# Kernel optimization log

Hardware: AMD Instinct MI355X
Metric: run time of the kernel (lower is better)

The kernel has to match this reference:

```python
import jax, jax.numpy as jnp
import numpy as np

B = 1024      # batch
V = 5023      # FLAME vertices
NF = 9976     # FLAME faces
NJ = 5        # joints: global, neck, jaw, eyeL, eyeR
NL = 51       # static landmarks
PARENTS = (-1, 0, 1, 1, 1)


def setup_inputs() -> dict:
    key = jax.random.key(0)
    ks = jax.random.split(key, 16)
    inp = {}
    # trainable flame parameters (small pose magnitudes for realism)
    inp['shape_params'] = jax.random.normal(ks[0], (B, 300), jnp.float32)
    inp['expression_params'] = jax.random.normal(ks[1], (B, 100), jnp.float32)
    inp['global_rot'] = 0.1 * jax.random.normal(ks[2], (B, 3), jnp.float32)
    inp['neck_pose'] = 0.1 * jax.random.normal(ks[3], (B, 3), jnp.float32)
    inp['jaw_pose'] = 0.1 * jax.random.normal(ks[4], (B, 3), jnp.float32)
    inp['eye_pose'] = 0.1 * jax.random.normal(ks[5], (B, 6), jnp.float32)
    inp['transl'] = jax.random.normal(ks[6], (B, 3), jnp.float32)
    # flame buffers
    inp['v_template'] = jax.random.normal(ks[7], (V, 3), jnp.float32)
    inp['shapedirs'] = 0.01 * jax.random.normal(ks[8], (V, 3, 400), jnp.float32)
    inp['posedirs'] = 0.01 * jax.random.normal(ks[9], (36, V * 3), jnp.float32)
    Jreg = jax.random.uniform(ks[10], (NJ, V), jnp.float32)
    inp['J_regressor'] = Jreg / jnp.sum(Jreg, axis=1, keepdims=True)
    W = jax.random.uniform(ks[11], (V, NJ), jnp.float32)
    inp['lbs_weights'] = W / jnp.sum(W, axis=1, keepdims=True)
    bc = jax.random.uniform(ks[12], (NL, 3), jnp.float32)
    inp['lmk_bary_coords'] = bc / jnp.sum(bc, axis=1, keepdims=True)
    inp['parents'] = jnp.array(PARENTS, dtype=jnp.int32)
    inp['faces'] = jax.random.randint(ks[13], (NF, 3), 0, V, jnp.int32)
    inp['lmk_faces_idx'] = jax.random.randint(ks[14], (NL,), 0, NF, jnp.int64)
    return inp


def batch_rodrigues(rvecs):
    # rvecs: [N,3] axis-angle -> [N,3,3] rotation matrices
    angle = jnp.sqrt(jnp.sum(jnp.square(rvecs + 1e-8), axis=1, keepdims=True))  # [N,1]
    axis = rvecs / angle
    s = jnp.sin(angle)[:, :, None]
    c = jnp.cos(angle)[:, :, None]
    rx, ry, rz = axis[:, 0], axis[:, 1], axis[:, 2]
    zeros = jnp.zeros_like(rx)
    K = jnp.stack([zeros, -rz, ry, rz, zeros, -rx, -ry, rx, zeros], axis=1).reshape(-1, 3, 3)
    I = jnp.eye(3, dtype=rvecs.dtype)
    return I + s * K + (1.0 - c) * (K @ K)


def _lbs(betas, full_pose, v_template, shapedirs, posedirs, J_regressor, lbs_weights):
    b = betas.shape[0]
    # shape+expression blendshapes
    v_shaped = v_template[None] + jnp.einsum('bl,vkl->bvk', betas, shapedirs)  # [B,V,3]
    joints = jnp.einsum('jv,bvk->bjk', J_regressor, v_shaped)                 # [B,J,3]
    rot_mats = batch_rodrigues(full_pose.reshape(-1, 3)).reshape(b, NJ, 3, 3)
    # pose blendshapes (exclude root)
    ident = jnp.eye(3, dtype=betas.dtype)
    pose_feature = (rot_mats[:, 1:] - ident).reshape(b, 9 * (NJ - 1))         # [B,36]
    v_posed = v_shaped + (pose_feature @ posedirs).reshape(b, V, 3)
    # rigid kinematic chain
    rel_joints = jnp.concatenate(
        [joints[:, :1], joints[:, 1:] - joints[:, jnp.array(PARENTS[1:])]], axis=1)
    bottom = jnp.broadcast_to(jnp.array([0., 0., 0., 1.], betas.dtype), (b, NJ, 1, 4))
    tf = jnp.concatenate(
        [jnp.concatenate([rot_mats, rel_joints[..., None]], axis=3), bottom], axis=2)  # [B,J,4,4]
    chain = [tf[:, 0]]
    for i in range(1, NJ):
        chain.append(chain[PARENTS[i]] @ tf[:, i])
    transforms = jnp.stack(chain, axis=1)                                    # [B,J,4,4]
    # remove rest-pose joint location from translation column
    jh = jnp.einsum('bjmn,bjn->bjm', transforms[:, :, :3, :3], joints)       # [B,J,3]
    A = transforms.at[:, :, :3, 3].add(-jh)
    # skinning
    T = jnp.einsum('vj,bjmn->bvmn', lbs_weights, A)                          # [B,V,4,4]
    v_h = jnp.concatenate([v_posed, jnp.ones((b, V, 1), betas.dtype)], axis=2)
    verts = jnp.einsum('bvmn,bvn->bvm', T, v_h)[..., :3]                     # [B,V,3]
    return verts, transforms[:, :, :3, 3]


def reference(shape_params, expression_params, global_rot, neck_pose, jaw_pose,
              eye_pose, transl, v_template, shapedirs, posedirs, J_regressor,
              lbs_weights, lmk_bary_coords, parents, faces, lmk_faces_idx):
    betas = jnp.concatenate([shape_params, expression_params], axis=1)       # [B,400]
    full_pose = jnp.concatenate([global_rot, neck_pose, jaw_pose, eye_pose], axis=1)  # [B,15]
    vertices, _ = _lbs(betas, full_pose, v_template, shapedirs, posedirs,
                       J_regressor, lbs_weights)
    # barycentric landmark interpolation
    lmk_faces = faces[lmk_faces_idx]                                         # [L,3]
    lmk_verts = vertices[:, lmk_faces]                                       # [B,L,3,3]
    landmarks_3d = jnp.einsum('blfk,lf->blk', lmk_verts, lmk_bary_coords)    # [B,L,3]
    landmarks_3d = landmarks_3d + transl[:, None]
    vertices = vertices + transl[:, None]
    # default-weights flame regularizer (fixed_shape=None, ref_vertices=None)
    flame_reg = (100.0 * jnp.sum(neck_pose ** 2)
                 + 0.001 * jnp.sum(jaw_pose ** 2)
                 + 0.001 * jnp.sum(shape_params ** 2)
                 + 0.001 * jnp.sum(expression_params ** 2))
    return vertices, landmarks_3d, flame_reg
```

## Files before the change

### kernel.cpp

```cpp
#include <hip/hip_runtime.h>
#include <hip/hip_bf16.h>

#define BATCH 1024
#define NV 5023
#define NJOINT 5
#define NLMK 51
#define N3 (NV*3)
#define NPADB 15072
#define KBETA 400
#define KTOT 448
#define NSTEP 14
#define RB_B (NPADB/16)
#define RB_A 64
#define FRAG 512

#define BM 64
#define BN 48
#define NVC 128
#define CVT_BLKS 3297

#define GBM 64
#define GBN 192
#define GNP 79
#define GGRID 1280
#define CH_S 52

typedef __attribute__((ext_vector_type(8))) short short8;
typedef __attribute__((ext_vector_type(4))) float floatx4;
typedef __attribute__((ext_vector_type(4))) float float4v;

#define GLDS16(gp, lp) \
    __builtin_amdgcn_global_load_lds( \
        (const __attribute__((address_space(1))) void*)(gp), \
        (__attribute__((address_space(3))) void*)(lp), 16, 0, 0)

#define WS_JS      0
#define WS_BASEJ   24064
#define WS_REG     24512
#define WS_FLAGS   24520
#define WS_AMAT    24576
#define WS_ACT     270336
#define WS_WB      1187840
#define WS_FULL    14692352

__device__ __forceinline__ float ldf(const void* p, long i, int f32) {
    if (f32) return ((const float*)p)[i];
    return __bfloat162float(((const __hip_bfloat16*)p)[i]);
}
__device__ __forceinline__ short8 ld8bf(const void* p, long i, int f32) {
    if (f32) {
        float4v a = *(const float4v*)((const float*)p + i);
        float4v b = *(const float4v*)((const float*)p + i + 4);
        short8 r;
#pragma unroll
        for (int j = 0; j < 4; ++j) {
            __hip_bfloat16 h = __float2bfloat16(a[j]);
            r[j] = *reinterpret_cast<short*>(&h);
        }
#pragma unroll
        for (int j = 0; j < 4; ++j) {
            __hip_bfloat16 h = __float2bfloat16(b[j]);
            r[4 + j] = *reinterpret_cast<short*>(&h);
        }
        return r;
    }
    return *(const short8*)((const __hip_bfloat16*)p + i);
}
__device__ __forceinline__ void stf(void* p, long i, float v, int f32) {
    if (f32) ((float*)p)[i] = v;
    else ((__hip_bfloat16*)p)[i] = __float2bfloat16(v);
}

__device__ __forceinline__ long act2_off(int b, int k) {
    return (((long)(k >> 5) * RB_A + (b >> 4)) * 64 + ((k >> 3) & 3) * 16 + (b & 15)) * 8 + (k & 7);
}

__device__ __forceinline__ int probe_f32(const void* shape_p) {
    int lane = threadIdx.x & 63;
    unsigned short h = ((const unsigned short*)shape_p)[2 * lane];
    union { unsigned short u; __hip_bfloat16 b; } cv; cv.u = h;
    float v = fabsf(__bfloat162float(cv.b));
    if (v != v) v = 3.4e38f;
#pragma unroll
    for (int off = 32; off; off >>= 1) v = fmaxf(v, __shfl_down(v, off));
    v = __shfl(v, 0);
    return v > 1e4f;
}
__device__ __forceinline__ int probe_i64(const void* lmk_idx) {
    int lane = threadIdx.x & 63;
    const int* q = (const int*)lmk_idx;
    int odd_nonzero = (lane < 25) && (q[2*lane + 1] != 0);
    unsigned long long b = __ballot(odd_nonzero);
    return b == 0ull;
}

__global__ void k_init(float* ws0, const void* shape_p, const void* lmk_idx, int* flags) {
    int i = blockIdx.x * 256 + threadIdx.x;
    if (i < 6129) ws0[i] = 0.f;
    if (blockIdx.x == 0 && threadIdx.x < 64) {
        int f = probe_f32(shape_p);
        int i64 = probe_i64(lmk_idx);
        if (threadIdx.x == 0) { flags[0] = f; flags[1] = i64; }
    }
}

__global__ __launch_bounds__(256) void k_prep(const void* __restrict__ shapedirs,
                                              const void* __restrict__ posedirs,
                                              const void* __restrict__ Jreg,
                                              const void* __restrict__ v_template,
                                              const void* __restrict__ shape_p,
                                              float* __restrict__ reg,
                                              __hip_bfloat16* __restrict__ Wb,
                                              float* __restrict__ PART) {
    int f32 = probe_f32(shape_p);
    int blk = blockIdx.x, tid = threadIdx.x;
    if (blk < CVT_BLKS) {
        if (blk == 0 && tid == 0) reg[0] = 0.f;
        int g = blk * 256 + tid;
        int s = g / (RB_B * 64);
        int rem = g - s * (RB_B * 64);
        int R = rem >> 6;
        int l = rem & 63;
        int quad = l >> 4, fr = l & 15;
        int n = R * 16 + fr;
        int k0 = s * 32 + quad * 8;
        short8 o;
#pragma unroll
        for (int e = 0; e < 8; ++e) o[e] = 0;
        if (n < N3) {
            if (k0 < KBETA) {
                o = ld8bf(shapedirs, (long)n * KBETA + k0, f32);
            } else if (k0 < 440) {
#pragma unroll
                for (int e = 0; e < 8; ++e) {
                    int kk = k0 + e - KBETA;
                    float val = (kk < 36) ? ldf(posedirs, (long)kk * N3 + n, f32) : 0.f;
                    __hip_bfloat16 h = __float2bfloat16(val);
                    o[e] = *reinterpret_cast<short*>(&h);
                }
            }
        }
        *(short8*)(Wb + (long)g * 8) = o;
    } else {
        int b2 = blk - CVT_BLKS;
        int k = b2 >> 7;
        int vc = b2 & 127;
        int v0 = vc * 40, v1 = min(NV, v0 + 40);
        int l2 = tid + 256;
        float acc1[NJOINT] = {0,0,0,0,0};
        float acc2[NJOINT] = {0,0,0,0,0};
        for (int v = v0; v < v1; ++v) {
            float s1 = ldf(shapedirs, (long)v*1200 + k*400 + tid, f32);
            float s2 = 0.f;
            if (l2 < 400)       s2 = ldf(shapedirs, (long)v*1200 + k*400 + l2, f32);
            else if (l2 == 400) s2 = ldf(v_template, v*3 + k, f32);
#pragma unroll
            for (int j = 0; j < NJOINT; ++j) {
                float jr = ldf(Jreg, j*NV + v, f32);
                acc1[j] += jr * s1;
                acc2[j] += jr * s2;
            }
        }
        long base = ((long)(k*NVC + vc)*5)*401;
#pragma unroll
        for (int j = 0; j < NJOINT; ++j) {
            PART[base + j*401 + tid] = acc1[j];
            if (l2 <= 400) PART[base + j*401 + l2] = acc2[j];
        }
    }
}

__global__ __launch_bounds__(256) void k_js_red(const float* __restrict__ PART,
                                                float* __restrict__ JS,
                                                float* __restrict__ baseJ) {
    int o = blockIdx.x * 256 + threadIdx.x;
    if (o >= 3*5*401) return;
    int k = o / 2005, r = o - k*2005;
    int j = r / 401, l = r - j*401;
    float s = 0.f;
    long base = ((long)(k*NVC)*5 + j)*401 + l;
    for (int vc = 0; vc < NVC; ++vc) s += PART[base + (long)vc*2005];
    if (l < 400) JS[j*1200 + k*400 + l] = s;
    else         baseJ[j*3 + k] = s;
}

__global__ void k_js_atomic(const void* __restrict__ Jreg,
                            const void* __restrict__ shapedirs,
                            const void* __restrict__ v_template,
                            const int* __restrict__ flags,
                            float* __restrict__ JS, float* __restrict__ baseJ) {
    int f32 = flags[0];
    int k = blockIdx.x, vc = blockIdx.y, tid = threadIdx.x;
    int v0 = vc * 79, v1 = min(NV, v0 + 79);
    int l2 = tid + 256;
    float acc1[NJOINT] = {0,0,0,0,0};
    float acc2[NJOINT] = {0,0,0,0,0};
    for (int v = v0; v < v1; ++v) {
        float s1 = ldf(shapedirs, (long)v*1200 + k*400 + tid, f32);
        float s2 = 0.f;
        if (l2 < 400)       s2 = ldf(shapedirs, (long)v*1200 + k*400 + l2, f32);
        else if (l2 == 400) s2 = ldf(v_template, v*3 + k, f32);
#pragma unroll
        for (int j = 0; j < NJOINT; ++j) {
            float jr = ldf(Jreg, j*NV + v, f32);
            acc1[j] += jr * s1;
            acc2[j] += jr * s2;
        }
    }
#pragma unroll
    for (int j = 0; j < NJOINT; ++j) {
        atomicAdd(&JS[j*1200 + k*400 + tid], acc1[j]);
        if (l2 < 400)       atomicAdd(&JS[j*1200 + k*400 + l2], acc2[j]);
        else if (l2 == 400) atomicAdd(&baseJ[j*3 + k], acc2[j]);
    }
}

__global__ __launch_bounds__(64) void k_batch(
        const void* __restrict__ shape_p, const void* __restrict__ expr_p,
        const void* __restrict__ grot, const void* __restrict__ neck,
        const void* __restrict__ jaw,  const void* __restrict__ eye,
        const float* __restrict__ JS, const float* __restrict__ baseJ,
        __hip_bfloat16* __restrict__ Act, float* __restrict__ Amat, float* __restrict__ reg) {
    int f32 = probe_f32(shape_p);
    int b = blockIdx.x, tid = threadIdx.x;
    __shared__ float betas[400];
    __shared__ float Rm[NJOINT][9];
    __shared__ float joints[NJOINT][3];
    __shared__ float Gm[NJOINT][12];

    for (int i = tid; i < 400; i += 64) {
        float v = (i < 300) ? ldf(shape_p, b*300 + i, f32)
                            : ldf(expr_p, b*100 + i - 300, f32);
        betas[i] = v;
        Act[act2_off(b, i)] = __float2bfloat16(v);
    }
    if (tid >= 36 && tid < 48) Act[act2_off(b, 400 + tid)] = __float2bfloat16(0.f);
    __syncthreads();

    if (tid < 60) {
        int o = tid % 15, q = tid / 15;
        int j = o / 3, kk = o - 3*j;
        const float* js = &JS[j*1200 + kk*400 + q*100];
        float s = 0.f;
        for (int l = 0; l < 100; ++l) s += js[l] * betas[q*100 + l];
        s += __shfl_down(s, 15);
        s += __shfl_down(s, 30);
        if (q == 0) joints[j][kk] = s + baseJ[o];
    }
    if (tid < NJOINT) {
        int j = tid;
        float r[3];
        for (int c = 0; c < 3; ++c) {
            if (j == 0)      r[c] = ldf(grot, b*3 + c, f32);
            else if (j == 1) r[c] = ldf(neck, b*3 + c, f32);
            else if (j == 2) r[c] = ldf(jaw,  b*3 + c, f32);
            else if (j == 3) r[c] = ldf(eye,  b*6 + c, f32);
            else             r[c] = ldf(eye,  b*6 + 3 + c, f32);
        }
        float a0 = r[0] + 1e-8f, a1 = r[1] + 1e-8f, a2 = r[2] + 1e-8f;
        float angle = sqrtf(a0*a0 + a1*a1 + a2*a2);
        float inv = 1.0f / angle;
        float rx = r[0]*inv, ry = r[1]*inv, rz = r[2]*inv;
        float s = sinf(angle), c = cosf(angle);
        float K[9] = {0.f, -rz, ry,  rz, 0.f, -rx,  -ry, rx, 0.f};
        float K2[9];
        for (int rr = 0; rr < 3; ++rr)
            for (int cc = 0; cc < 3; ++cc) {
                float t = 0.f;
                for (int m = 0; m < 3; ++m) t += K[rr*3+m] * K[m*3+cc];
                K2[rr*3+cc] = t;
            }
        for (int i2 = 0; i2 < 9; ++i2) {
            float id = (i2 == 0 || i2 == 4 || i2 == 8) ? 1.f : 0.f;
            Rm[j][i2] = id + s*K[i2] + (1.f - c)*K2[i2];
        }
    }
    __syncthreads();

    if (tid < 36) {
        int i = tid / 9 + 1, rc = tid - (tid/9)*9;
        float id = (rc == 0 || rc == 4 || rc == 8) ? 1.f : 0.f;
        Act[act2_off(b, 400 + tid)] = __float2bfloat16(Rm[i][rc] - id);
    }
    if (tid == 0) {
        for (int rr = 0; rr < 3; ++rr) {
            for (int cc = 0; cc < 3; ++cc) Gm[0][rr*4+cc] = Rm[0][rr*3+cc];
            Gm[0][rr*4+3] = joints[0][rr];
        }
        const int par[NJOINT] = {-1, 0, 1, 1, 1};
        for (int j = 1; j < NJOINT; ++j) {
            int p = par[j];
            float rel[3];
            for (int c2 = 0; c2 < 3; ++c2) rel[c2] = joints[j][c2] - joints[p][c2];
            for (int rr = 0; rr < 3; ++rr) {
                for (int cc = 0; cc < 3; ++cc) {
                    float t = 0.f;
                    for (int m = 0; m < 3; ++m) t += Gm[p][rr*4+m] * Rm[j][m*3+cc];
                    Gm[j][rr*4+cc] = t;
                }
                float t = Gm[p][rr*4+3];
                for (int m = 0; m < 3; ++m) t += Gm[p][rr*4+m] * rel[m];
                Gm[j][rr*4+3] = t;
            }
        }
    }
    __syncthreads();

    if (tid < 60) {
        int j = tid / 12, e = tid - j*12, rr = e / 4, cc = e - rr*4;
        float val = Gm[j][e];
        if (cc == 3)
            for (int m = 0; m < 3; ++m) val -= Gm[j][rr*4+m] * joints[j][m];
        Amat[b*60 + tid] = val;
    }

    float part = 0.f;
    for (int i = tid; i < 400; i += 64) part += betas[i]*betas[i];
    part *= 0.001f;
    if (tid == 0) {
        float nn = 0.f, jj = 0.f;
        for (int c = 0; c < 3; ++c) {
            float nv = ldf(neck, b*3+c, f32);
            float jv = ldf(jaw,  b*3+c, f32);
            nn += nv*nv; jj += jv*jv;
        }
        part += 100.f*nn + 0.001f*jj;
    }
    for (int off = 32; off; off >>= 1) part += __shfl_down(part, off);
    if (tid == 0) atomicAdd(reg, part);
}

__global__ __launch_bounds__(512, 2) void k_gemm_lbs_big(
        const __hip_bfloat16* __restrict__ Act,
        const __hip_bfloat16* __restrict__ Wb,
        const void* __restrict__ v_template,
        const float* __restrict__ Amat,
        const void* __restrict__ weights,
        const void* __restrict__ transl,
        const void* __restrict__ shape_p,
        void* __restrict__ out) {
    __shared__ __align__(16) __hip_bfloat16 stage[2][16 * FRAG];
    __shared__ float chunk[8][16 * CH_S];
    __shared__ float Al[GBM * 60];
    __shared__ float wl[64 * 5];
    __shared__ float tl[GBM * 3];
    __shared__ float vtl[GBN];

    int f32 = probe_f32(shape_p);
    int tid = threadIdx.x;
    int wave = tid >> 6, lane = tid & 63;
    int fr = lane & 15, quad = lane >> 4;
    int mg = wave >> 2, wn = wave & 3;

    int lin = blockIdx.x;
    int xcd = lin & 7, slot = lin >> 3;
    int P = (slot >> 4) * 8 + xcd;
    int mblk = slot & 15;
    if (P >= GNP) return;
    int m0 = mblk * GBM;
    int v0 = P * 64;

    for (int i = tid; i < GBM*60/4; i += 512)
        ((float4v*)Al)[i] = ((const float4v*)(Amat + (long)m0*60))[i];
    if (tid < 320) {
        int v = v0 + tid / 5;
        wl[tid] = (v < NV) ? ldf(weights, v*5 + tid % 5, f32) : 0.f;
    }
    if (tid < GBM*3)
        tl[tid] = ldf(transl, (long)m0*3 + tid, f32);
    if (tid >= 320) {
        int i = tid - 320;
        vtl[i] = ((long)v0*3 + i < N3) ? ldf(v_template, (long)v0*3 + i, f32) : 0.f;
    }

    int r0 = wave*2, r1 = wave*2 + 1;
    long aoff0 = 0, aoff1 = 0;
    const __hip_bfloat16* base0;
    const __hip_bfloat16* base1;
    int sstr0, sstr1;
    {
        if (r0 < 4) { base0 = Act; sstr0 = RB_A; aoff0 = mblk*4 + r0; }
        else {
            long rb = (long)P*12 + (r0 - 4);
            if (rb > RB_B-1) rb = RB_B-1;
            base0 = Wb; sstr0 = RB_B; aoff0 = rb;
        }
        if (r1 < 4) { base1 = Act; sstr1 = RB_A; aoff1 = mblk*4 + r1; }
        else {
            long rb = (long)P*12 + (r1 - 4);
            if (rb > RB_B-1) rb = RB_B-1;
            base1 = Wb; sstr1 = RB_B; aoff1 = rb;
        }
    }
    __hip_bfloat16* lds0[2] = { &stage[0][r0*FRAG], &stage[1][r0*FRAG] };
    __hip_bfloat16* lds1[2] = { &stage[0][r1*FRAG], &stage[1][r1*FRAG] };

    floatx4 acc[2][3];
#pragma unroll
    for (int q = 0; q < 2; ++q)
#pragma unroll
        for (int t = 0; t < 3; ++t) acc[q][t] = (floatx4){0.f,0.f,0.f,0.f};

    asm volatile("s_waitcnt vmcnt(0)" ::: "memory");
    __builtin_amdgcn_sched_barrier(0);
    GLDS16(base0 + ((long)0*sstr0 + aoff0)*FRAG + lane*8, lds0[0]);
    GLDS16(base1 + ((long)0*sstr1 + aoff1)*FRAG + lane*8, lds1[0]);
    GLDS16(base0 + ((long)1*sstr0 + aoff0)*FRAG + lane*8, lds0[1]);
    GLDS16(base1 + ((long)1*sstr1 + aoff1)*FRAG + lane*8, lds1[1]);

#pragma unroll
    for (int s = 0; s < NSTEP; ++s) {
        const int cb = s & 1;
        if (s == NSTEP-1) { asm volatile("s_waitcnt vmcnt(0)" ::: "memory"); }
        else              { asm volatile("s_waitcnt vmcnt(2)" ::: "memory"); }
        __builtin_amdgcn_sched_barrier(0);
        __builtin_amdgcn_s_barrier();
        __builtin_amdgcn_sched_barrier(0);
        const __hip_bfloat16* sb = stage[cb];
        short8 a0 = *(const short8*)&sb[(mg*2 + 0)*FRAG + lane*8];
        short8 a1 = *(const short8*)&sb[(mg*2 + 1)*FRAG + lane*8];
        short8 b0 = *(const short8*)&sb[(4 + wn*3 + 0)*FRAG + lane*8];
        short8 b1 = *(const short8*)&sb[(4 + wn*3 + 1)*FRAG + lane*8];
        short8 b2 = *(const short8*)&sb[(4 + wn*3 + 2)*FRAG + lane*8];
        acc[0][0] = __builtin_amdgcn_mfma_f32_16x16x32_bf16(a0, b0, acc[0][0], 0, 0, 0);
        acc[0][1] = __builtin_amdgcn_mfma_f32_16x16x32_bf16(a0, b1, acc[0][1], 0, 0, 0);
        acc[0][2] = __builtin_amdgcn_mfma_f32_16x16x32_bf16(a0, b2, acc[0][2], 0, 0, 0);
        acc[1][0] = __builtin_amdgcn_mfma_f32_16x16x32_bf16(a1, b0, acc[1][0], 0, 0, 0);
        acc[1][1] = __builtin_amdgcn_mfma_f32_16x16x32_bf16(a1, b1, acc[1][1], 0, 0, 0);
        acc[1][2] = __builtin_amdgcn_mfma_f32_16x16x32_bf16(a1, b2, acc[1][2], 0, 0, 0);
        __builtin_amdgcn_sched_barrier(0);
        __builtin_amdgcn_s_barrier();
        __builtin_amdgcn_sched_barrier(0);
        if (s + 2 < NSTEP) {
            GLDS16(base0 + ((long)(s+2)*sstr0 + aoff0)*FRAG + lane*8, lds0[cb]);
            GLDS16(base1 + ((long)(s+2)*sstr1 + aoff1)*FRAG + lane*8, lds1[cb]);
        }
    }

    __syncthreads();
    float* ch = chunk[wave];
    int mloc = lane >> 2, vq = lane & 3;
#pragma unroll
    for (int q = 0; q < 2; ++q) {
#pragma unroll
        for (int t = 0; t < 3; ++t)
#pragma unroll
            for (int rr = 0; rr < 4; ++rr)
                ch[(quad*4 + rr)*CH_S + t*16 + fr] = acc[q][t][rr];
        __syncthreads();
        int mb = mg*32 + q*16 + mloc;
        long mglob = m0 + mb;
        const float* A = &Al[mb*60];
        float t0c = tl[mb*3+0], t1c = tl[mb*3+1], t2c = tl[mb*3+2];
        long obase = (mglob*NV + v0)*3;
#pragma unroll
        for (int vi = 0; vi < 4; ++vi) {
            int vloc = wn*16 + vq*4 + vi;
            int v = v0 + vloc;
            if (v < NV) {
                int o = mloc*CH_S + (vq*4 + vi)*3;
                float p0 = ch[o+0] + vtl[vloc*3 + 0];
                float p1 = ch[o+1] + vtl[vloc*3 + 1];
                float p2 = ch[o+2] + vtl[vloc*3 + 2];
                float w0 = wl[vloc*5+0], w1 = wl[vloc*5+1], w2 = wl[vloc*5+2];
                float w3 = wl[vloc*5+3], w4 = wl[vloc*5+4];
#pragma unroll
                for (int c = 0; c < 3; ++c) {
                    float t0 = w0*A[c*4+0] + w1*A[12+c*4+0] + w2*A[24+c*4+0] + w3*A[36+c*4+0] + w4*A[48+c*4+0];
                    float t1 = w0*A[c*4+1] + w1*A[12+c*4+1] + w2*A[24+c*4+1] + w3*A[36+c*4+1] + w4*A[48+c*4+1];
                    float t2 = w0*A[c*4+2] + w1*A[12+c*4+2] + w2*A[24+c*4+2] + w3*A[36+c*4+2] + w4*A[48+c*4+2];
                    float t3 = w0*A[c*4+3] + w1*A[12+c*4+3] + w2*A[24+c*4+3] + w3*A[36+c*4+3] + w4*A[48+c*4+3];
                    float tlc = (c == 0) ? t0c : ((c == 1) ? t1c : t2c);
                    float val = t0*p0 + t1*p1 + t2*p2 + t3 + tlc;
                    stf(out, obase + vloc*3 + c, val, f32);
                }
            }
        }
        __syncthreads();
    }
}

__global__ __launch_bounds__(256) void k_gemm_lbs_small(
        const __hip_bfloat16* __restrict__ Act,
        const void* __restrict__ shapedirs,
        const void* __restrict__ posedirs,
        const void* __restrict__ v_template,
        const float* __restrict__ Amat,
        const void* __restrict__ weights,
        const void* __restrict__ transl,
        const int* __restrict__ flags,
        void* __restrict__ out) {
    __shared__ float tileS[4][16*49 + 4];
    __shared__ float AlS[4][960];
    __shared__ float wl[80];
    __shared__ __align__(16) __hip_bfloat16 Bs2[BN * 64];

    int f32 = flags[0];
    int tid = threadIdx.x;
    int wave = tid >> 6, lane = tid & 63;
    int fr = lane & 15, quad = lane >> 4;
    int m0 = blockIdx.x * 256;
    int n0 = blockIdx.y * BN;
    int v0 = blockIdx.y * 16;

    if (tid < 80) {
        int v = v0 + tid / 5;
        wl[tid] = (v < NV) ? ldf(weights, v*5 + tid % 5, f32) : 0.f;
    }
    for (int i = tid; i < BN * 64; i += 256) {
        int n = i >> 6, kk = i & 63;
        int nc = min(n0 + n, N3 - 1);
        float val = 0.f;
        if (kk < 16)      val = ldf(shapedirs, (long)nc*KBETA + 384 + kk, f32);
        else if (kk < 52) val = ldf(posedirs, (long)(kk-16)*N3 + nc, f32);
        Bs2[n*64 + kk] = __float2bfloat16(val);
    }
    __syncthreads();

    int Ra0 = (m0 >> 4) + wave*4;
    int nr[3];
#pragma unroll
    for (int t = 0; t < 3; ++t) nr[t] = min(n0 + t*16 + fr, N3 - 1);

    floatx4 acc[4][3];
#pragma unroll
    for (int sub = 0; sub < 4; ++sub)
#pragma unroll
        for (int t = 0; t < 3; ++t) acc[sub][t] = (floatx4){0.f,0.f,0.f,0.f};

#pragma unroll
    for (int s = 0; s < 14; ++s) {
        short8 bb[3];
#pragma unroll
        for (int t = 0; t < 3; ++t) {
            if (s < 12) bb[t] = ld8bf(shapedirs, (long)nr[t]*KBETA + s*32 + quad*8, f32);
            else        bb[t] = *(short8*)&Bs2[(t*16 + fr)*64 + (s-12)*32 + quad*8];
        }
#pragma unroll
        for (int sub = 0; sub < 4; ++sub) {
            short8 a = *(const short8*)(Act + (((long)s*RB_A + Ra0 + sub)*64 + lane)*8);
#pragma unroll
            for (int t = 0; t < 3; ++t)
                acc[sub][t] = __builtin_amdgcn_mfma_f32_16x16x32_bf16(a, bb[t], acc[sub][t], 0, 0, 0);
        }
    }

    int vloc = fr, rgrp = quad;
    int v = v0 + vloc;
    float tpl0 = 0.f, tpl1 = 0.f, tpl2 = 0.f;
    if (v < NV) {
        tpl0 = ldf(v_template, v*3 + 0, f32);
        tpl1 = ldf(v_template, v*3 + 1, f32);
        tpl2 = ldf(v_template, v*3 + 2, f32);
    }
    float w0 = wl[vloc*5+0], w1 = wl[vloc*5+1], w2 = wl[vloc*5+2];
    float w3 = wl[vloc*5+3], w4 = wl[vloc*5+4];
    for (int sub = 0; sub < 4; ++sub) {
#pragma unroll
        for (int t = 0; t < 3; ++t)
#pragma unroll
            for (int rr = 0; rr < 4; ++rr)
                tileS[wave][(quad*4 + rr)*49 + t*16 + fr] = acc[sub][t][rr];
        for (int i = lane; i < 960; i += 64)
            AlS[wave][i] = Amat[(long)(m0 + wave*64 + sub*16)*60 + i];
        __syncthreads();
        if (v < NV) {
#pragma unroll
            for (int rr = 0; rr < 4; ++rr) {
                int mloc = rgrp*4 + rr;
                long m = m0 + wave*64 + sub*16 + mloc;
                float p0 = tileS[wave][mloc*49 + vloc*3 + 0] + tpl0;
                float p1 = tileS[wave][mloc*49 + vloc*3 + 1] + tpl1;
                float p2 = tileS[wave][mloc*49 + vloc*3 + 2] + tpl2;
                const float* A = &AlS[wave][mloc*60];
#pragma unroll
                for (int c = 0; c < 3; ++c) {
                    float t0 = w0*A[c*4+0] + w1*A[12+c*4+0] + w2*A[24+c*4+0] + w3*A[36+c*4+0] + w4*A[48+c*4+0];
                    float t1 = w0*A[c*4+1] + w1*A[12+c*4+1] + w2*A[24+c*4+1] + w3*A[36+c*4+1] + w4*A[48+c*4+1];
                    float t2 = w0*A[c*4+2] + w1*A[12+c*4+2] + w2*A[24+c*4+2] + w3*A[36+c*4+2] + w4*A[48+c*4+2];
                    float t3 = w0*A[c*4+3] + w1*A[12+c*4+3] + w2*A[24+c*4+3] + w3*A[36+c*4+3] + w4*A[48+c*4+3];
                    float val = t0*p0 + t1*p1 + t2*p2 + t3 + ldf(transl, m*3 + c, f32);
                    stf(out, (m*NV + v)*3 + c, val, f32);
                }
            }
        }
        __syncthreads();
    }
}

__global__ __launch_bounds__(64) void k_lmk(const void* __restrict__ verts,
                                            const void* __restrict__ bary,
                                            const int* __restrict__ faces,
                                            const void* __restrict__ lmk_idx,
                                            const void* __restrict__ transl,
                                            const float* __restrict__ reg,
                                            const void* __restrict__ shape_p,
                                            void* __restrict__ out) {
    int f32 = probe_f32(shape_p);
    int i64 = probe_i64(lmk_idx);
    int b = blockIdx.x, tid = threadIdx.x;
    if (b == 0 && tid == 63)
        stf(out, (long)BATCH*NV*3 + (long)BATCH*NLMK*3, reg[0], f32);
    if (tid >= NLMK) return;
    int f = i64 ? (int)((const long long*)lmk_idx)[tid]
                : ((const int*)lmk_idx)[tid];
    float acc[3] = {0.f, 0.f, 0.f};
    float bsum = 0.f;
    for (int fi = 0; fi < 3; ++fi) {
        int vi = faces[f*3 + fi];
        float bc = ldf(bary, tid*3 + fi, f32);
        bsum += bc;
#pragma unroll
        for (int c = 0; c < 3; ++c)
            acc[c] += bc * ldf(verts, ((long)b*NV + vi)*3 + c, f32);
    }
#pragma unroll
    for (int c = 0; c < 3; ++c) {
        float val = acc[c] + (1.f - bsum) * ldf(transl, b*3 + c, f32);
        stf(out, (long)BATCH*NV*3 + ((long)b*NLMK + tid)*3 + c, val, f32);
    }
}

extern "C" void kernel_launch(void* const* d_in, const int* in_sizes, int n_in,
                              void* d_out, int out_size, void* d_ws, size_t ws_size,
                              hipStream_t stream) {
    const void* shape_p   = d_in[0];
    const void* expr_p    = d_in[1];
    const void* grot      = d_in[2];
    const void* neck      = d_in[3];
    const void* jaw       = d_in[4];
    const void* eye       = d_in[5];
    const void* transl    = d_in[6];
    const void* v_templ   = d_in[7];
    const void* shapedirs = d_in[8];
    const void* posedirs  = d_in[9];
    const void* Jreg      = d_in[10];
    const void* weights   = d_in[11];
    const void* bary      = d_in[12];
    const int*  faces     = (const int*)d_in[14];
    const void* lmk_idx   = d_in[15];

    char* ws = (char*)d_ws;
    float* JS      = (float*)(ws + WS_JS);
    float* baseJ   = (float*)(ws + WS_BASEJ);
    float* reg     = (float*)(ws + WS_REG);
    int*   flags   = (int*)(ws + WS_FLAGS);
    float* Amat    = (float*)(ws + WS_AMAT);
    __hip_bfloat16* Act = (__hip_bfloat16*)(ws + WS_ACT);
    __hip_bfloat16* Wb  = (__hip_bfloat16*)(ws + WS_WB);
    float* PART    = (float*)d_out;
    bool big = ws_size >= (size_t)WS_FULL;

    if (big) {
        k_prep<<<CVT_BLKS + 384, 256, 0, stream>>>(shapedirs, posedirs, Jreg, v_templ,
                                                   shape_p, reg, Wb, PART);
        k_js_red<<<24, 256, 0, stream>>>(PART, JS, baseJ);
    } else {
        k_init<<<24, 256, 0, stream>>>((float*)ws, shape_p, lmk_idx, flags);
        k_js_atomic<<<dim3(3, 64), 256, 0, stream>>>(Jreg, shapedirs, v_templ, flags, JS, baseJ);
    }
    k_batch<<<BATCH, 64, 0, stream>>>(shape_p, expr_p, grot, neck, jaw, eye,
                                      JS, baseJ, Act, Amat, reg);
    if (big) {
        k_gemm_lbs_big<<<GGRID, 512, 0, stream>>>(Act, Wb, v_templ, Amat,
                                                  weights, transl, shape_p, d_out);
    } else {
        dim3 grid(BATCH/256, (N3 + BN - 1)/BN);
        k_gemm_lbs_small<<<grid, 256, 0, stream>>>(Act, shapedirs, posedirs, v_templ,
                                                   Amat, weights, transl, flags, d_out);
    }
    k_lmk<<<BATCH, 64, 0, stream>>>(d_out, bary, faces, lmk_idx, transl, reg, shape_p, d_out);
}
```

Baseline: 263.2 us.

## Restructure prep kernel: coalesced shapedirs reads, separate pose packing, finer JS partials

The weight-packing pass now maps threads along the contiguous shapedirs row so each thread reads consecutive 16-byte chunks and scatters them into the MFMA fragment layout, rather than gathering by output order. Posedirs packing gets its own block range that touches only the pose columns. The joint-shape reduction uses 360 vertex chunks of 14 instead of 128 of 40, giving more parallel blocks, and stages J_regressor values in shared memory. The cost is a larger partial-sum buffer and a longer serial loop in the follow-up reduction kernel.

```diff
diff --git a/kernel.cpp b/kernel.cpp
--- a/kernel.cpp
+++ b/kernel.cpp
@@ -16,8 +16,14 @@
 
 #define BM 64
 #define BN 48
-#define NVC 128
-#define CVT_BLKS 3297
+
+#define PK_BETA_CH (NPADB*50)
+#define PK_BETA_BLKS 2944
+#define PK_POSE_CH (RB_B*96)
+#define PK_POSE_BLKS 354
+#define NVC2 360
+#define VCH 14
+#define PK_JS_BLKS (3*NVC2)
 
 #define GBM 64
 #define GBN 192
@@ -112,56 +118,71 @@
                                               float* __restrict__ reg,
                                               __hip_bfloat16* __restrict__ Wb,
                                               float* __restrict__ PART) {
+    __shared__ float jl[NJOINT * VCH];
     int f32 = probe_f32(shape_p);
     int blk = blockIdx.x, tid = threadIdx.x;
-    if (blk < CVT_BLKS) {
+    if (blk < PK_BETA_BLKS) {
         if (blk == 0 && tid == 0) reg[0] = 0.f;
         int g = blk * 256 + tid;
-        int s = g / (RB_B * 64);
-        int rem = g - s * (RB_B * 64);
-        int R = rem >> 6;
-        int l = rem & 63;
-        int quad = l >> 4, fr = l & 15;
+        if (g >= PK_BETA_CH) return;
+        int n = g / 50, kg = g - n * 50;
+        short8 o;
+#pragma unroll
+        for (int e = 0; e < 8; ++e) o[e] = 0;
+        if (n < N3) o = ld8bf(shapedirs, (long)n * KBETA + kg * 8, f32);
+        long chunk = ((long)(kg >> 2) * RB_B + (n >> 4)) * 64 + (kg & 3) * 16 + (n & 15);
+        *(short8*)(Wb + chunk * 8) = o;
+    } else if (blk < PK_BETA_BLKS + PK_POSE_BLKS) {
+        int g = (blk - PK_BETA_BLKS) * 256 + tid;
+        if (g >= PK_POSE_CH) return;
+        int R = g / 96, rem = g - R * 96;
+        int c = rem >> 4, fr = rem & 15;
         int n = R * 16 + fr;
-        int k0 = s * 32 + quad * 8;
+        int k0 = KBETA + 8 * c;
         short8 o;
 #pragma unroll
         for (int e = 0; e < 8; ++e) o[e] = 0;
         if (n < N3) {
-            if (k0 < KBETA) {
-                o = ld8bf(shapedirs, (long)n * KBETA + k0, f32);
-            } else if (k0 < 440) {
-#pragma unroll
-                for (int e = 0; e < 8; ++e) {
-                    int kk = k0 + e - KBETA;
-                    float val = (kk < 36) ? ldf(posedirs, (long)kk * N3 + n, f32) : 0.f;
-                    __hip_bfloat16 h = __float2bfloat16(val);
-                    o[e] = *reinterpret_cast<short*>(&h);
-                }
+#pragma unroll
+            for (int e = 0; e < 8; ++e) {
+                int kk = k0 + e - KBETA;
+                float val = (kk < 36) ? ldf(posedirs, (long)kk * N3 + n, f32) : 0.f;
+                __hip_bfloat16 h = __float2bfloat16(val);
+                o[e] = *reinterpret_cast<short*>(&h);
             }
         }
-        *(short8*)(Wb + (long)g * 8) = o;
+        long chunk = ((long)(k0 >> 5) * RB_B + R) * 64 + ((k0 >> 3) & 3) * 16 + fr;
+        *(short8*)(Wb + chunk * 8) = o;
     } else {
-        int b2 = blk - CVT_BLKS;
-        int k = b2 >> 7;
-        int vc = b2 & 127;
-        int v0 = vc * 40, v1 = min(NV, v0 + 40);
+        int b2 = blk - (PK_BETA_BLKS + PK_POSE_BLKS);
+        int k = b2 / NVC2;
+        int vc = b2 - k * NVC2;
+        int v0 = vc * VCH;
+        if (tid < NJOINT * VCH) {
+            int j = tid / VCH, i = tid - j * VCH;
+            int v = min(v0 + i, NV - 1);
+            jl[tid] = ldf(Jreg, (long)j * NV + v, f32);
+        }
+        __syncthreads();
         int l2 = tid + 256;
         float acc1[NJOINT] = {0,0,0,0,0};
         float acc2[NJOINT] = {0,0,0,0,0};
-        for (int v = v0; v < v1; ++v) {
+#pragma unroll
+        for (int i = 0; i < VCH; ++i) {
+            int v = v0 + i;
+            if (v >= NV) break;
             float s1 = ldf(shapedirs, (long)v*1200 + k*400 + tid, f32);
             float s2 = 0.f;
             if (l2 < 400)       s2 = ldf(shapedirs, (long)v*1200 + k*400 + l2, f32);
             else if (l2 == 400) s2 = ldf(v_template, v*3 + k, f32);
 #pragma unroll
             for (int j = 0; j < NJOINT; ++j) {
-                float jr = ldf(Jreg, j*NV + v, f32);
+                float jr = jl[j*VCH + i];
                 acc1[j] += jr * s1;
                 acc2[j] += jr * s2;
             }
         }
-        long base = ((long)(k*NVC + vc)*5)*401;
+        long base = ((long)(k*NVC2 + vc)*5)*401;
 #pragma unroll
         for (int j = 0; j < NJOINT; ++j) {
             PART[base + j*401 + tid] = acc1[j];
@@ -178,8 +199,8 @@
     int k = o / 2005, r = o - k*2005;
     int j = r / 401, l = r - j*401;
     float s = 0.f;
-    long base = ((long)(k*NVC)*5 + j)*401 + l;
-    for (int vc = 0; vc < NVC; ++vc) s += PART[base + (long)vc*2005];
+    long base = ((long)(k*NVC2)*5 + j)*401 + l;
+    for (int vc = 0; vc < NVC2; ++vc) s += PART[base + (long)vc*2005];
     if (l < 400) JS[j*1200 + k*400 + l] = s;
     else         baseJ[j*3 + k] = s;
 }
@@ -652,8 +673,8 @@
     bool big = ws_size >= (size_t)WS_FULL;
 
     if (big) {
-        k_prep<<<CVT_BLKS + 384, 256, 0, stream>>>(shapedirs, posedirs, Jreg, v_templ,
-                                                   shape_p, reg, Wb, PART);
+        k_prep<<<PK_BETA_BLKS + PK_POSE_BLKS + PK_JS_BLKS, 256, 0, stream>>>(
+            shapedirs, posedirs, Jreg, v_templ, shape_p, reg, Wb, PART);
         k_js_red<<<24, 256, 0, stream>>>(PART, JS, baseJ);
     } else {
         k_init<<<24, 256, 0, stream>>>((float*)ws, shape_p, lmk_idx, flags);
```

Result: faster. 254.5 us (-3.3%).
